# Kernel optimization log

Hardware: AMD Instinct MI355X
Metric: run time of the kernel (lower is better)

The kernel has to match this reference:

```python
import jax, jax.numpy as jnp
import numpy as np

N, E = 50000, 800000
DIN, DH, DOUT, L = 128, 256, 64, 4


def setup_inputs() -> dict:
    key = jax.random.key(0)
    ks = jax.random.split(key, 8)
    x = jax.random.normal(ks[0], (N, DIN), dtype=jnp.float32)
    edge_index = jax.random.randint(ks[1], (2, E), 0, N, dtype=jnp.int64 if jax.config.jax_enable_x64 else jnp.int32)
    W_emb = jax.random.normal(ks[2], (DIN, DH), dtype=jnp.float32) / np.float32(np.sqrt(DIN))
    b_emb = jnp.zeros((DH,), jnp.float32)
    W_conv = jax.random.normal(ks[3], (L, DH, DH), dtype=jnp.float32) / np.float32(np.sqrt(DH))
    b_conv = jnp.zeros((L, DH), jnp.float32)
    W_out = jax.random.normal(ks[4], (DH, DOUT), dtype=jnp.float32) / np.float32(np.sqrt(DH))
    b_out = jnp.zeros((DOUT,), jnp.float32)
    return {"x": x, "edge_index": edge_index, "W_emb": W_emb, "b_emb": b_emb,
            "W_conv": W_conv, "b_conv": b_conv, "W_out": W_out, "b_out": b_out}


def _gcn_layer(h, src, dst, norm, W, b, n):
    # GCNConv: transform, then sym-normalized neighbor aggregation, then bias
    h = h @ W                                  # [N, DH]
    msg = h[src] * norm[:, None]               # [E+N, DH] gather + scale
    return jax.ops.segment_sum(msg, dst, num_segments=n) + b


def reference(x, edge_index, W_emb, b_emb, W_conv, b_conv, W_out, b_out):
    n = x.shape[0]
    loop = jnp.arange(n, dtype=edge_index.dtype)
    src = jnp.concatenate([edge_index[0], loop])   # add self-loops (PyG default)
    dst = jnp.concatenate([edge_index[1], loop])
    deg = jax.ops.segment_sum(jnp.ones_like(src, dtype=x.dtype), dst, num_segments=n)
    dinv = jnp.where(deg > 0, jax.lax.rsqrt(deg), jnp.zeros_like(deg))
    norm = dinv[src] * dinv[dst]                   # per-edge D^-1/2 A D^-1/2 weight
    h = x @ W_emb + b_emb                          # embedding (no activation)
    for i in range(L):                             # small fixed layer count
        h = jnp.tanh(_gcn_layer(h, src, dst, norm, W_conv[i], b_conv[i], n))
    return h @ W_out + b_out
```

## Files before the change

kernel.cpp:

```cpp
#include <hip/hip_runtime.h>
#include <math.h>

#define N_NODES 50000
#define N_EDGES 800000
#define DIN 128
#define DH 256
#define DOUT 64
#define NLAYERS 4

typedef unsigned short u16;
typedef __attribute__((ext_vector_type(8))) short short8;
typedef __attribute__((ext_vector_type(4))) float f32x4;

__device__ inline u16 f2bf(float f) {
  unsigned int u = __float_as_uint(f);
  u += 0x7fff + ((u >> 16) & 1);
  return (u16)(u >> 16);
}
__device__ inline float bf2f(u16 h) {
  return __uint_as_float(((unsigned int)h) << 16);
}

#define GLD16(gp, lp)                                                        \
  __builtin_amdgcn_global_load_lds(                                          \
      (const __attribute__((address_space(1))) void*)(const void*)(gp),      \
      (__attribute__((address_space(3))) void*)(void*)(lp), 16, 0, 0)


__global__ void k_count(const int* __restrict__ dst, int* __restrict__ cnt, int e) {
  int i = blockIdx.x * blockDim.x + threadIdx.x;
  if (i < e) atomicAdd(&cnt[dst[i]], 1);
}

__global__ void k_scan1(const int* __restrict__ cnt, int* __restrict__ rowptr,
                        int* __restrict__ bsum, float* __restrict__ dinv, int n) {
  __shared__ int sm[256];
  int i = blockIdx.x * 256 + threadIdx.x;
  int v = (i < n) ? cnt[i] : 0;
  if (i < n) dinv[i] = rsqrtf((float)v + 1.0f);
  sm[threadIdx.x] = v;
  __syncthreads();
  for (int off = 1; off < 256; off <<= 1) {
    int t = (threadIdx.x >= off) ? sm[threadIdx.x - off] : 0;
    __syncthreads();
    sm[threadIdx.x] += t;
    __syncthreads();
  }
  if (i < n) rowptr[i + 1] = sm[threadIdx.x];
  if (threadIdx.x == 255) bsum[blockIdx.x] = sm[255];
}

__global__ void k_scan2(int* bsum, int nb) {
  __shared__ int sm[256];
  int v = (threadIdx.x < nb) ? bsum[threadIdx.x] : 0;
  sm[threadIdx.x] = v;
  __syncthreads();
  for (int off = 1; off < 256; off <<= 1) {
    int t = (threadIdx.x >= off) ? sm[threadIdx.x - off] : 0;
    __syncthreads();
    sm[threadIdx.x] += t;
    __syncthreads();
  }
  if (threadIdx.x < nb) bsum[threadIdx.x] = sm[threadIdx.x] - v;
}

__global__ void k_scan3(int* __restrict__ rowptr, const int* __restrict__ bsum,
                        int* __restrict__ cursor, int n) {
  int i = blockIdx.x * 256 + threadIdx.x;
  if (i < n) {
    int v = rowptr[i + 1] + bsum[blockIdx.x];
    rowptr[i + 1] = v;
    if (i + 1 < n) cursor[i + 1] = v;
  }
  if (blockIdx.x == 0 && threadIdx.x == 0) {
    rowptr[0] = 0;
    cursor[0] = 0;
  }
}

__global__ void k_fill(const int* __restrict__ src, const int* __restrict__ dst,
                       const float* __restrict__ dinv,
                       int* __restrict__ cursor, int2* __restrict__ csr, int e) {
  int i = blockIdx.x * blockDim.x + threadIdx.x;
  if (i < e) {
    int d = dst[i], s = src[i];
    int pos = atomicAdd(&cursor[d], 1);
    csr[pos] = make_int2(s, __float_as_int(dinv[s] * dinv[d]));
  }
}


__global__ void k_f2bf4(const float* __restrict__ in, u16* __restrict__ out, int n4) {
  int i = blockIdx.x * 256 + threadIdx.x;
  if (i < n4) {
    float4 v = ((const float4*)in)[i];
    ushort4 o;
    o.x = f2bf(v.x); o.y = f2bf(v.y); o.z = f2bf(v.z); o.w = f2bf(v.w);
    ((ushort4*)out)[i] = o;
  }
}

#define W_EMB_SZ (DIN * DH)
#define W_CONV_SZ (DH * DH)
#define W_OUT_SZ (3 * DH * DOUT)
__global__ void k_weights(const float* __restrict__ W_emb, const float* __restrict__ W_conv,
                          const float* __restrict__ W_out, u16* __restrict__ Bt_emb,
                          u16* __restrict__ Bt_conv, u16* __restrict__ Bt_out) {
  int i = blockIdx.x * 256 + threadIdx.x;
  if (i < W_EMB_SZ) {
    int n = i >> 7, k = i & (DIN - 1);
    Bt_emb[i] = f2bf(W_emb[k * DH + n]);
  } else if (i < W_EMB_SZ + 4 * W_CONV_SZ) {
    int j = i - W_EMB_SZ;
    int l = j >> 16, jj = j & (W_CONV_SZ - 1);
    int n = jj >> 8, k = jj & (DH - 1);
    Bt_conv[j] = f2bf(W_conv[l * W_CONV_SZ + k * DH + n]);
  } else if (i < W_EMB_SZ + 4 * W_CONV_SZ + W_OUT_SZ) {
    int j = i - W_EMB_SZ - 4 * W_CONV_SZ;
    int n = j / (3 * DH), kp = j % (3 * DH);
    int k = (kp < DH) ? kp : ((kp < 2 * DH) ? kp - DH : kp - 2 * DH);
    float wv = W_out[k * DOUT + n];
    u16 hiv = f2bf(wv);
    u16 v = hiv;
    if (kp >= DH && kp < 2 * DH) v = f2bf(wv - bf2f(hiv));
    Bt_out[j] = v;
  }
}

template <int BN, int NSPLIT, int EPI>
__global__ __launch_bounds__(256) void k_gemm_mfma(
    const u16* __restrict__ Ahi, const u16* __restrict__ Alo,
    const u16* __restrict__ Bt, const float* __restrict__ bias,
    float* __restrict__ Cf, u16* __restrict__ Cb, int M, int K, int N) {
  constexpr int BM = 128, BK = 64;
  constexpr int WN = BN / 2;
  constexpr int NT = WN / 16;
  constexpr int BNG = BN / 16;
  __shared__ u16 As[2 * 8 * 512];
  __shared__ u16 Bs[2 * BNG * 512];
  const int tid = threadIdx.x;
  const int w = tid >> 6, lane = tid & 63;
  const int q = lane >> 4, r = lane & 15;
  const int wmg = (w >> 1) * 4;
  const int wng = (w & 1) * NT;
  const int m0 = blockIdx.x * BM, n0 = blockIdx.y * BN;
  const int Kp = NSPLIT * K;
  const int srow = lane & 15;
  const int sk = (lane >> 4) * 8;

  f32x4 acc[4][NT];
#pragma unroll
  for (int t = 0; t < 4; t++)
#pragma unroll
    for (int u = 0; u < NT; u++) acc[t][u] = (f32x4){0.f, 0.f, 0.f, 0.f};

  for (int k0 = 0; k0 < Kp; k0 += BK) {
    const u16* Aptr;
    int ka;
    if (NSPLIT == 1) {
      Aptr = Ahi; ka = k0;
    } else {
      Aptr = (k0 < 2 * K) ? Ahi : Alo;
      ka = (k0 < K) ? k0 : ((k0 < 2 * K) ? (k0 - K) : (k0 - 2 * K));
    }
#pragma unroll
    for (int ii = 0; ii < 4; ii++) {
      int g = w * 2 + (ii & 1), kb = ii >> 1;
      int grow = m0 + g * 16 + srow;
      if (grow > M - 1) grow = M - 1;
      const u16* gp = Aptr + (size_t)grow * K + ka + kb * 32 + sk;
      GLD16(gp, &As[(kb * 8 + g) * 512] + (size_t)lane * 8);
    }
#pragma unroll
    for (int ii = 0; ii < BN / 32; ii++) {
      int g, kb;
      if (BN == 128) { g = w * 2 + (ii & 1); kb = ii >> 1; }
      else { g = w; kb = ii; }
      const u16* gp = Bt + (size_t)(n0 + g * 16 + srow) * Kp + k0 + kb * 32 + sk;
      GLD16(gp, &Bs[(kb * BNG + g) * 512] + (size_t)lane * 8);
    }
    __syncthreads();
#pragma unroll
    for (int kb = 0; kb < 2; kb++) {
      short8 af[4], bfr[NT];
#pragma unroll
      for (int t = 0; t < 4; t++)
        af[t] = *(const short8*)&As[((kb * 8 + wmg + t) * 64 + lane) * 8];
#pragma unroll
      for (int u = 0; u < NT; u++)
        bfr[u] = *(const short8*)&Bs[((kb * BNG + wng + u) * 64 + lane) * 8];
#pragma unroll
      for (int t = 0; t < 4; t++)
#pragma unroll
        for (int u = 0; u < NT; u++)
          acc[t][u] = __builtin_amdgcn_mfma_f32_16x16x32_bf16(af[t], bfr[u], acc[t][u], 0, 0, 0);
    }
    __syncthreads();
  }

#pragma unroll
  for (int t = 0; t < 4; t++) {
#pragma unroll
    for (int rg = 0; rg < 4; rg++) {
      int row = m0 + (w >> 1) * 64 + t * 16 + q * 4 + rg;
      if (row < M) {
#pragma unroll
        for (int u = 0; u < NT; u++) {
          int col = n0 + (w & 1) * WN + u * 16 + r;
          float v = acc[t][u][rg];
          if (bias) v += bias[col];
          if (EPI == 0)
            Cf[(size_t)row * N + col] = v;
          else
            Cb[(size_t)row * N + col] = f2bf(v);
        }
      }
    }
  }
}

__global__ void k_aggregate(const u16* __restrict__ tmpb,
                            const int* __restrict__ rowptr, const int2* __restrict__ csr,
                            const float* __restrict__ dinv, const float* __restrict__ bias,
                            u16* __restrict__ hi, u16* __restrict__ lo, int n) {
  int i = (int)((blockIdx.x * (size_t)blockDim.x + threadIdx.x) >> 6);
  int lane = threadIdx.x & 63;
  if (i >= n) return;
  float w0 = dinv[i];
  w0 *= w0;
  const ushort4* T = (const ushort4*)tmpb;
  float4 bv = ((const float4*)bias)[lane];
  ushort4 t0 = T[(size_t)i * 64 + lane];
  float ax = bv.x + w0 * bf2f(t0.x);
  float ay = bv.y + w0 * bf2f(t0.y);
  float az = bv.z + w0 * bf2f(t0.z);
  float aw = bv.w + w0 * bf2f(t0.w);
  int s = rowptr[i], e = rowptr[i + 1];
  int j = s;
  for (; j + 4 <= e; j += 4) {
    int2 c0 = csr[j], c1 = csr[j + 1], c2 = csr[j + 2], c3 = csr[j + 3];
    ushort4 v0 = T[(size_t)c0.x * 64 + lane];
    ushort4 v1 = T[(size_t)c1.x * 64 + lane];
    ushort4 v2 = T[(size_t)c2.x * 64 + lane];
    ushort4 v3 = T[(size_t)c3.x * 64 + lane];
    float f0 = __int_as_float(c0.y), f1 = __int_as_float(c1.y);
    float f2 = __int_as_float(c2.y), f3 = __int_as_float(c3.y);
    ax += f0 * bf2f(v0.x); ay += f0 * bf2f(v0.y); az += f0 * bf2f(v0.z); aw += f0 * bf2f(v0.w);
    ax += f1 * bf2f(v1.x); ay += f1 * bf2f(v1.y); az += f1 * bf2f(v1.z); aw += f1 * bf2f(v1.w);
    ax += f2 * bf2f(v2.x); ay += f2 * bf2f(v2.y); az += f2 * bf2f(v2.z); aw += f2 * bf2f(v2.w);
    ax += f3 * bf2f(v3.x); ay += f3 * bf2f(v3.y); az += f3 * bf2f(v3.z); aw += f3 * bf2f(v3.w);
  }
  for (; j < e; j++) {
    int2 c = csr[j];
    ushort4 v = T[(size_t)c.x * 64 + lane];
    float f = __int_as_float(c.y);
    ax += f * bf2f(v.x); ay += f * bf2f(v.y); az += f * bf2f(v.z); aw += f * bf2f(v.w);
  }
  float ox = tanhf(ax), oy = tanhf(ay), oz = tanhf(az), ow = tanhf(aw);
  size_t base = (size_t)i * DH + lane * 4;
  ushort4 hv;
  hv.x = f2bf(ox); hv.y = f2bf(oy); hv.z = f2bf(oz); hv.w = f2bf(ow);
  *(ushort4*)(hi + base) = hv;
  if (lo) {
    ushort4 lv;
    lv.x = f2bf(ox - bf2f(hv.x));
    lv.y = f2bf(oy - bf2f(hv.y));
    lv.z = f2bf(oz - bf2f(hv.z));
    lv.w = f2bf(ow - bf2f(hv.w));
    *(ushort4*)(lo + base) = lv;
  }
}


extern "C" void kernel_launch(void* const* d_in, const int* in_sizes, int n_in,
                              void* d_out, int out_size, void* d_ws, size_t ws_size,
                              hipStream_t stream) {
  const float* x = (const float*)d_in[0];
  const int* eidx = (const int*)d_in[1];
  const int* esrc = eidx;
  const int* edst = eidx + N_EDGES;
  const float* W_emb = (const float*)d_in[2];
  const float* b_emb = (const float*)d_in[3];
  const float* W_conv = (const float*)d_in[4];
  const float* b_conv = (const float*)d_in[5];
  const float* W_out = (const float*)d_in[6];
  const float* b_out = (const float*)d_in[7];
  float* out = (float*)d_out;

  char* ws = (char*)d_ws;
  size_t off = 0;
  auto alloc = [&](size_t bytes) -> void* {
    void* p = ws + off;
    off += (bytes + 255) & ~(size_t)255;
    return p;
  };
  u16* tmpb = (u16*)alloc((size_t)N_NODES * DH * 2);
  u16* h_hi = (u16*)alloc((size_t)N_NODES * DH * 2);
  u16* h_lo = (u16*)alloc((size_t)N_NODES * DH * 2);
  u16* x_bf = h_lo;
  float* dinv = (float*)alloc((size_t)N_NODES * 4);
  int* cnt = (int*)alloc((size_t)N_NODES * 4);
  int* rowptr = (int*)alloc((size_t)(N_NODES + 1) * 4);
  int* cursor = (int*)alloc((size_t)N_NODES * 4);
  int* bsum = (int*)alloc((size_t)((N_NODES + 255) / 256) * 4);
  int2* csr = (int2*)alloc((size_t)N_EDGES * 8);
  u16* Bt_emb = (u16*)alloc((size_t)W_EMB_SZ * 2);
  u16* Bt_conv = (u16*)alloc((size_t)4 * W_CONV_SZ * 2);
  u16* Bt_out = (u16*)alloc((size_t)W_OUT_SZ * 2);

  int nb = (N_NODES + 255) / 256;
  int eb = (N_EDGES + 255) / 256;

  hipMemsetAsync(cnt, 0, (size_t)N_NODES * 4, stream);
  k_count<<<eb, 256, 0, stream>>>(edst, cnt, N_EDGES);
  k_scan1<<<nb, 256, 0, stream>>>(cnt, rowptr, bsum, dinv, N_NODES);
  k_scan2<<<1, 256, 0, stream>>>(bsum, nb);
  k_scan3<<<nb, 256, 0, stream>>>(rowptr, bsum, cursor, N_NODES);
  k_fill<<<eb, 256, 0, stream>>>(esrc, edst, dinv, cursor, csr, N_EDGES);

  k_f2bf4<<<(N_NODES * DIN / 4 + 255) / 256, 256, 0, stream>>>(x, x_bf, N_NODES * DIN / 4);
  {
    int tot = W_EMB_SZ + 4 * W_CONV_SZ + W_OUT_SZ;
    k_weights<<<(tot + 255) / 256, 256, 0, stream>>>(W_emb, W_conv, W_out,
                                                     Bt_emb, Bt_conv, Bt_out);
  }

  int mblocks = (N_NODES + 127) / 128;
  int aggblocks = (N_NODES * 64 + 255) / 256;

  {
    dim3 g(mblocks, DH / 128);
    k_gemm_mfma<128, 1, 1><<<g, 256, 0, stream>>>(x_bf, nullptr, Bt_emb, b_emb,
                                                  nullptr, h_hi, N_NODES, DIN, DH);
  }
  for (int l = 0; l < NLAYERS; l++) {
    dim3 g(mblocks, DH / 128);
    k_gemm_mfma<128, 1, 1><<<g, 256, 0, stream>>>(h_hi, nullptr,
                                                  Bt_conv + (size_t)l * W_CONV_SZ, nullptr,
                                                  nullptr, tmpb, N_NODES, DH, DH);
    k_aggregate<<<aggblocks, 256, 0, stream>>>(tmpb, rowptr, csr, dinv,
                                               b_conv + (size_t)l * DH,
                                               h_hi, (l == 3) ? h_lo : nullptr, N_NODES);
  }
  {
    dim3 g(mblocks, 1);
    k_gemm_mfma<64, 3, 0><<<g, 256, 0, stream>>>(h_hi, h_lo, Bt_out, b_out,
                                                 out, nullptr, N_NODES, DH, DOUT);
  }
}
```

Before: 572.1 us.

## Switch to fp16, use LDS-free per-wave GEMM, fuse conversion kernels, unroll aggregation

Moves all intermediate storage and MFMA inputs from bf16 to fp16. The LDS-staged block GEMM is replaced by a per-wave 64x64 tile GEMM that loads operands straight from global memory, which removes the barriers and LDS traffic but loses cross-wave reuse. The input and weight conversion kernels are merged into one launch, and the aggregation gather loop is unrolled by 8 to keep more loads in flight. fp16 has a narrower range than bf16, which could overflow on unusual inputs, though tanh-bounded activations limit that risk.

```diff
diff --git a/kernel.cpp b/kernel.cpp
--- a/kernel.cpp
+++ b/kernel.cpp
@@ -9,22 +9,17 @@
 #define NLAYERS 4
 
 typedef unsigned short u16;
-typedef __attribute__((ext_vector_type(8))) short short8;
+typedef __attribute__((ext_vector_type(8))) _Float16 half8;
 typedef __attribute__((ext_vector_type(4))) float f32x4;
 
-__device__ inline u16 f2bf(float f) {
-  unsigned int u = __float_as_uint(f);
-  u += 0x7fff + ((u >> 16) & 1);
-  return (u16)(u >> 16);
-}
-__device__ inline float bf2f(u16 h) {
-  return __uint_as_float(((unsigned int)h) << 16);
-}
-
-#define GLD16(gp, lp)                                                        \
-  __builtin_amdgcn_global_load_lds(                                          \
-      (const __attribute__((address_space(1))) void*)(const void*)(gp),      \
-      (__attribute__((address_space(3))) void*)(void*)(lp), 16, 0, 0)
+__device__ inline u16 f2h(float f) {
+  _Float16 h = (_Float16)f;
+  return *(u16*)&h;
+}
+__device__ inline float h2f(u16 u) {
+  _Float16 h = *(_Float16*)&u;
+  return (float)h;
+}
 
 
 __global__ void k_count(const int* __restrict__ dst, int* __restrict__ cnt, int e) {
@@ -89,137 +84,119 @@
   }
 }
 
-
-__global__ void k_f2bf4(const float* __restrict__ in, u16* __restrict__ out, int n4) {
-  int i = blockIdx.x * 256 + threadIdx.x;
-  if (i < n4) {
-    float4 v = ((const float4*)in)[i];
-    ushort4 o;
-    o.x = f2bf(v.x); o.y = f2bf(v.y); o.z = f2bf(v.z); o.w = f2bf(v.w);
-    ((ushort4*)out)[i] = o;
-  }
-}
-
+#define X_Q (N_NODES * DIN / 4)
 #define W_EMB_SZ (DIN * DH)
 #define W_CONV_SZ (DH * DH)
 #define W_OUT_SZ (3 * DH * DOUT)
-__global__ void k_weights(const float* __restrict__ W_emb, const float* __restrict__ W_conv,
+#define W_TOT (W_EMB_SZ + 4 * W_CONV_SZ + W_OUT_SZ)
+
+__global__ void k_convert(const float* __restrict__ x, u16* __restrict__ x_f16,
+                          const float* __restrict__ W_emb, const float* __restrict__ W_conv,
                           const float* __restrict__ W_out, u16* __restrict__ Bt_emb,
                           u16* __restrict__ Bt_conv, u16* __restrict__ Bt_out) {
   int i = blockIdx.x * 256 + threadIdx.x;
-  if (i < W_EMB_SZ) {
-    int n = i >> 7, k = i & (DIN - 1);
-    Bt_emb[i] = f2bf(W_emb[k * DH + n]);
-  } else if (i < W_EMB_SZ + 4 * W_CONV_SZ) {
-    int j = i - W_EMB_SZ;
+  if (i < X_Q) {
+    float4 v = ((const float4*)x)[i];
+    ushort4 o;
+    o.x = f2h(v.x); o.y = f2h(v.y); o.z = f2h(v.z); o.w = f2h(v.w);
+    ((ushort4*)x_f16)[i] = o;
+    return;
+  }
+  int t = i - X_Q;
+  if (t < W_EMB_SZ) {
+    int n = t >> 7, k = t & (DIN - 1);
+    Bt_emb[t] = f2h(W_emb[k * DH + n]);
+  } else if (t < W_EMB_SZ + 4 * W_CONV_SZ) {
+    int j = t - W_EMB_SZ;
     int l = j >> 16, jj = j & (W_CONV_SZ - 1);
     int n = jj >> 8, k = jj & (DH - 1);
-    Bt_conv[j] = f2bf(W_conv[l * W_CONV_SZ + k * DH + n]);
-  } else if (i < W_EMB_SZ + 4 * W_CONV_SZ + W_OUT_SZ) {
-    int j = i - W_EMB_SZ - 4 * W_CONV_SZ;
+    Bt_conv[j] = f2h(W_conv[l * W_CONV_SZ + k * DH + n]);
+  } else if (t < W_TOT) {
+    int j = t - W_EMB_SZ - 4 * W_CONV_SZ;
     int n = j / (3 * DH), kp = j % (3 * DH);
     int k = (kp < DH) ? kp : ((kp < 2 * DH) ? kp - DH : kp - 2 * DH);
     float wv = W_out[k * DOUT + n];
-    u16 hiv = f2bf(wv);
+    u16 hiv = f2h(wv);
     u16 v = hiv;
-    if (kp >= DH && kp < 2 * DH) v = f2bf(wv - bf2f(hiv));
+    if (kp >= DH && kp < 2 * DH) v = f2h(wv - h2f(hiv));
     Bt_out[j] = v;
   }
 }
 
-template <int BN, int NSPLIT, int EPI>
-__global__ __launch_bounds__(256) void k_gemm_mfma(
+template <int NSPLIT, int EPI>
+__global__ __launch_bounds__(256) void k_gemm_direct(
     const u16* __restrict__ Ahi, const u16* __restrict__ Alo,
     const u16* __restrict__ Bt, const float* __restrict__ bias,
     float* __restrict__ Cf, u16* __restrict__ Cb, int M, int K, int N) {
-  constexpr int BM = 128, BK = 64;
-  constexpr int WN = BN / 2;
-  constexpr int NT = WN / 16;
-  constexpr int BNG = BN / 16;
-  __shared__ u16 As[2 * 8 * 512];
-  __shared__ u16 Bs[2 * BNG * 512];
-  const int tid = threadIdx.x;
-  const int w = tid >> 6, lane = tid & 63;
+  const int lane = threadIdx.x & 63;
+  const int w = threadIdx.x >> 6;
   const int q = lane >> 4, r = lane & 15;
-  const int wmg = (w >> 1) * 4;
-  const int wng = (w & 1) * NT;
-  const int m0 = blockIdx.x * BM, n0 = blockIdx.y * BN;
+  const int ntiles = N >> 6;
+  const int mtiles = (M + 63) >> 6;
+  int waveId = blockIdx.x * 4 + w;
+  if (waveId >= mtiles * ntiles) return;
+  int ntile = waveId % ntiles;
+  int mtile = waveId / ntiles;
+  const int m0 = mtile * 64, n0 = ntile * 64;
   const int Kp = NSPLIT * K;
-  const int srow = lane & 15;
-  const int sk = (lane >> 4) * 8;
-
-  f32x4 acc[4][NT];
+
+  int rowA[4];
+#pragma unroll
+  for (int t = 0; t < 4; t++) {
+    int rr = m0 + t * 16 + r;
+    rowA[t] = (rr < M) ? rr : (M - 1);
+  }
+
+  f32x4 acc[4][4];
 #pragma unroll
   for (int t = 0; t < 4; t++)
 #pragma unroll
-    for (int u = 0; u < NT; u++) acc[t][u] = (f32x4){0.f, 0.f, 0.f, 0.f};
-
-  for (int k0 = 0; k0 < Kp; k0 += BK) {
-    const u16* Aptr;
-    int ka;
-    if (NSPLIT == 1) {
-      Aptr = Ahi; ka = k0;
-    } else {
-      Aptr = (k0 < 2 * K) ? Ahi : Alo;
-      ka = (k0 < K) ? k0 : ((k0 < 2 * K) ? (k0 - K) : (k0 - 2 * K));
+    for (int u = 0; u < 4; u++) acc[t][u] = (f32x4){0.f, 0.f, 0.f, 0.f};
+
+  for (int s = 0; s < NSPLIT; s++) {
+    const u16* Aseg = (s == 2) ? Alo : Ahi;
+    const u16* Bseg = Bt + s * K;
+    for (int kk = 0; kk < K; kk += 32) {
+      half8 af[4], bfr[4];
+#pragma unroll
+      for (int t = 0; t < 4; t++)
+        af[t] = *(const half8*)(Aseg + (size_t)rowA[t] * K + kk + q * 8);
+#pragma unroll
+      for (int u = 0; u < 4; u++)
+        bfr[u] = *(const half8*)(Bseg + (size_t)(n0 + u * 16 + r) * Kp + kk + q * 8);
+#pragma unroll
+      for (int t = 0; t < 4; t++)
+#pragma unroll
+        for (int u = 0; u < 4; u++)
+          acc[t][u] = __builtin_amdgcn_mfma_f32_16x16x32_f16(af[t], bfr[u], acc[t][u], 0, 0, 0);
     }
-#pragma unroll
-    for (int ii = 0; ii < 4; ii++) {
-      int g = w * 2 + (ii & 1), kb = ii >> 1;
-      int grow = m0 + g * 16 + srow;
-      if (grow > M - 1) grow = M - 1;
-      const u16* gp = Aptr + (size_t)grow * K + ka + kb * 32 + sk;
-      GLD16(gp, &As[(kb * 8 + g) * 512] + (size_t)lane * 8);
-    }
-#pragma unroll
-    for (int ii = 0; ii < BN / 32; ii++) {
-      int g, kb;
-      if (BN == 128) { g = w * 2 + (ii & 1); kb = ii >> 1; }
-      else { g = w; kb = ii; }
-      const u16* gp = Bt + (size_t)(n0 + g * 16 + srow) * Kp + k0 + kb * 32 + sk;
-      GLD16(gp, &Bs[(kb * BNG + g) * 512] + (size_t)lane * 8);
-    }
-    __syncthreads();
-#pragma unroll
-    for (int kb = 0; kb < 2; kb++) {
-      short8 af[4], bfr[NT];
-#pragma unroll
-      for (int t = 0; t < 4; t++)
-        af[t] = *(const short8*)&As[((kb * 8 + wmg + t) * 64 + lane) * 8];
-#pragma unroll
-      for (int u = 0; u < NT; u++)
-        bfr[u] = *(const short8*)&Bs[((kb * BNG + wng + u) * 64 + lane) * 8];
-#pragma unroll
-      for (int t = 0; t < 4; t++)
-#pragma unroll
-        for (int u = 0; u < NT; u++)
-          acc[t][u] = __builtin_amdgcn_mfma_f32_16x16x32_bf16(af[t], bfr[u], acc[t][u], 0, 0, 0);
-    }
-    __syncthreads();
-  }
+  }
+
+  float bv[4];
+#pragma unroll
+  for (int u = 0; u < 4; u++) bv[u] = bias ? bias[n0 + u * 16 + r] : 0.f;
 
 #pragma unroll
   for (int t = 0; t < 4; t++) {
 #pragma unroll
     for (int rg = 0; rg < 4; rg++) {
-      int row = m0 + (w >> 1) * 64 + t * 16 + q * 4 + rg;
+      int row = m0 + t * 16 + q * 4 + rg;
       if (row < M) {
 #pragma unroll
-        for (int u = 0; u < NT; u++) {
-          int col = n0 + (w & 1) * WN + u * 16 + r;
-          float v = acc[t][u][rg];
-          if (bias) v += bias[col];
+        for (int u = 0; u < 4; u++) {
+          int col = n0 + u * 16 + r;
+          float v = acc[t][u][rg] + bv[u];
           if (EPI == 0)
             Cf[(size_t)row * N + col] = v;
           else
-            Cb[(size_t)row * N + col] = f2bf(v);
+            Cb[(size_t)row * N + col] = f2h(v);
         }
       }
     }
   }
 }
 
-__global__ void k_aggregate(const u16* __restrict__ tmpb,
+__global__ void k_aggregate(const u16* __restrict__ tmph,
                             const int* __restrict__ rowptr, const int2* __restrict__ csr,
                             const float* __restrict__ dinv, const float* __restrict__ bias,
                             u16* __restrict__ hi, u16* __restrict__ lo, int n) {
@@ -228,45 +205,67 @@
   if (i >= n) return;
   float w0 = dinv[i];
   w0 *= w0;
-  const ushort4* T = (const ushort4*)tmpb;
+  const ushort4* T = (const ushort4*)tmph;
   float4 bv = ((const float4*)bias)[lane];
   ushort4 t0 = T[(size_t)i * 64 + lane];
-  float ax = bv.x + w0 * bf2f(t0.x);
-  float ay = bv.y + w0 * bf2f(t0.y);
-  float az = bv.z + w0 * bf2f(t0.z);
-  float aw = bv.w + w0 * bf2f(t0.w);
+  float ax = bv.x + w0 * h2f(t0.x);
+  float ay = bv.y + w0 * h2f(t0.y);
+  float az = bv.z + w0 * h2f(t0.z);
+  float aw = bv.w + w0 * h2f(t0.w);
   int s = rowptr[i], e = rowptr[i + 1];
   int j = s;
+  for (; j + 8 <= e; j += 8) {
+    int2 c[8];
+    ushort4 v[8];
+#pragma unroll
+    for (int u = 0; u < 8; u++) c[u] = csr[j + u];
+#pragma unroll
+    for (int u = 0; u < 8; u++) v[u] = T[(size_t)c[u].x * 64 + lane];
+#pragma unroll
+    for (int u = 0; u < 8; u++) {
+      float f = __int_as_float(c[u].y);
+      ax += f * h2f(v[u].x);
+      ay += f * h2f(v[u].y);
+      az += f * h2f(v[u].z);
+      aw += f * h2f(v[u].w);
+    }
+  }
   for (; j + 4 <= e; j += 4) {
-    int2 c0 = csr[j], c1 = csr[j + 1], c2 = csr[j + 2], c3 = csr[j + 3];
-    ushort4 v0 = T[(size_t)c0.x * 64 + lane];
-    ushort4 v1 = T[(size_t)c1.x * 64 + lane];
-    ushort4 v2 = T[(size_t)c2.x * 64 + lane];
-    ushort4 v3 = T[(size_t)c3.x * 64 + lane];
-    float f0 = __int_as_float(c0.y), f1 = __int_as_float(c1.y);
-    float f2 = __int_as_float(c2.y), f3 = __int_as_float(c3.y);
-    ax += f0 * bf2f(v0.x); ay += f0 * bf2f(v0.y); az += f0 * bf2f(v0.z); aw += f0 * bf2f(v0.w);
-    ax += f1 * bf2f(v1.x); ay += f1 * bf2f(v1.y); az += f1 * bf2f(v1.z); aw += f1 * bf2f(v1.w);
-    ax += f2 * bf2f(v2.x); ay += f2 * bf2f(v2.y); az += f2 * bf2f(v2.z); aw += f2 * bf2f(v2.w);
-    ax += f3 * bf2f(v3.x); ay += f3 * bf2f(v3.y); az += f3 * bf2f(v3.z); aw += f3 * bf2f(v3.w);
+    int2 c[4];
+    ushort4 v[4];
+#pragma unroll
+    for (int u = 0; u < 4; u++) c[u] = csr[j + u];
+#pragma unroll
+    for (int u = 0; u < 4; u++) v[u] = T[(size_t)c[u].x * 64 + lane];
+#pragma unroll
+    for (int u = 0; u < 4; u++) {
+      float f = __int_as_float(c[u].y);
+      ax += f * h2f(v[u].x);
+      ay += f * h2f(v[u].y);
+      az += f * h2f(v[u].z);
+      aw += f * h2f(v[u].w);
+    }
   }
   for (; j < e; j++) {
     int2 c = csr[j];
     ushort4 v = T[(size_t)c.x * 64 + lane];
     float f = __int_as_float(c.y);
-    ax += f * bf2f(v.x); ay += f * bf2f(v.y); az += f * bf2f(v.z); aw += f * bf2f(v.w);
+    ax += f * h2f(v.x);
+    ay += f * h2f(v.y);
+    az += f * h2f(v.z);
+    aw += f * h2f(v.w);
   }
   float ox = tanhf(ax), oy = tanhf(ay), oz = tanhf(az), ow = tanhf(aw);
   size_t base = (size_t)i * DH + lane * 4;
   ushort4 hv;
-  hv.x = f2bf(ox); hv.y = f2bf(oy); hv.z = f2bf(oz); hv.w = f2bf(ow);
+  hv.x = f2h(ox); hv.y = f2h(oy); hv.z = f2h(oz); hv.w = f2h(ow);
   *(ushort4*)(hi + base) = hv;
   if (lo) {
     ushort4 lv;
-    lv.x = f2bf(ox - bf2f(hv.x));
-    lv.y = f2bf(oy - bf2f(hv.y));
-    lv.z = f2bf(oz - bf2f(hv.z));
-    lv.w = f2bf(ow - bf2f(hv.w));
+    lv.x = f2h(ox - h2f(hv.x));
+    lv.y = f2h(oy - h2f(hv.y));
+    lv.z = f2h(oz - h2f(hv.z));
+    lv.w = f2h(ow - h2f(hv.w));
     *(ushort4*)(lo + base) = lv;
   }
 }
@@ -294,10 +293,10 @@
     off += (bytes + 255) & ~(size_t)255;
     return p;
   };
-  u16* tmpb = (u16*)alloc((size_t)N_NODES * DH * 2);
+  u16* tmph = (u16*)alloc((size_t)N_NODES * DH * 2);
   u16* h_hi = (u16*)alloc((size_t)N_NODES * DH * 2);
   u16* h_lo = (u16*)alloc((size_t)N_NODES * DH * 2);
-  u16* x_bf = h_lo;
+  u16* x_f16 = h_lo;
   float* dinv = (float*)alloc((size_t)N_NODES * 4);
   int* cnt = (int*)alloc((size_t)N_NODES * 4);
   int* rowptr = (int*)alloc((size_t)(N_NODES + 1) * 4);
@@ -317,34 +316,22 @@
   k_scan2<<<1, 256, 0, stream>>>(bsum, nb);
   k_scan3<<<nb, 256, 0, stream>>>(rowptr, bsum, cursor, N_NODES);
   k_fill<<<eb, 256, 0, stream>>>(esrc, edst, dinv, cursor, csr, N_EDGES);
-
-  k_f2bf4<<<(N_NODES * DIN / 4 + 255) / 256, 256, 0, stream>>>(x, x_bf, N_NODES * DIN / 4);
-  {
-    int tot = W_EMB_SZ + 4 * W_CONV_SZ + W_OUT_SZ;
-    k_weights<<<(tot + 255) / 256, 256, 0, stream>>>(W_emb, W_conv, W_out,
-                                                     Bt_emb, Bt_conv, Bt_out);
-  }
-
-  int mblocks = (N_NODES + 127) / 128;
+  k_convert<<<(X_Q + W_TOT + 255) / 256, 256, 0, stream>>>(x, x_f16, W_emb, W_conv, W_out,
+                                                           Bt_emb, Bt_conv, Bt_out);
+
+  int mtiles = (N_NODES + 63) / 64;
   int aggblocks = (N_NODES * 64 + 255) / 256;
 
-  {
-    dim3 g(mblocks, DH / 128);
-    k_gemm_mfma<128, 1, 1><<<g, 256, 0, stream>>>(x_bf, nullptr, Bt_emb, b_emb,
-                                                  nullptr, h_hi, N_NODES, DIN, DH);
-  }
+  k_gemm_direct<1, 1><<<(mtiles * (DH / 64) + 3) / 4, 256, 0, stream>>>(
+      x_f16, nullptr, Bt_emb, b_emb, nullptr, h_hi, N_NODES, DIN, DH);
   for (int l = 0; l < NLAYERS; l++) {
-    dim3 g(mblocks, DH / 128);
-    k_gemm_mfma<128, 1, 1><<<g, 256, 0, stream>>>(h_hi, nullptr,
-                                                  Bt_conv + (size_t)l * W_CONV_SZ, nullptr,
-                                                  nullptr, tmpb, N_NODES, DH, DH);
-    k_aggregate<<<aggblocks, 256, 0, stream>>>(tmpb, rowptr, csr, dinv,
+    k_gemm_direct<1, 1><<<(mtiles * (DH / 64) + 3) / 4, 256, 0, stream>>>(
+        h_hi, nullptr, Bt_conv + (size_t)l * W_CONV_SZ, nullptr,
+        nullptr, tmph, N_NODES, DH, DH);
+    k_aggregate<<<aggblocks, 256, 0, stream>>>(tmph, rowptr, csr, dinv,
                                                b_conv + (size_t)l * DH,
                                                h_hi, (l == 3) ? h_lo : nullptr, N_NODES);
   }
-  {
-    dim3 g(mblocks, 1);
-    k_gemm_mfma<64, 3, 0><<<g, 256, 0, stream>>>(h_hi, h_lo, Bt_out, b_out,
-                                                 out, nullptr, N_NODES, DH, DOUT);
-  }
-}
+  k_gemm_direct<3, 0><<<(mtiles * (DOUT / 64) + 3) / 4, 256, 0, stream>>>(
+      h_hi, h_lo, Bt_out, b_out, out, nullptr, N_NODES, DH, DOUT);
+}
```

Result: slower. 612.3 us (+7.0%).
